# Kernel tuning notes

Measured on AMD Instinct MI355X. Metric: run time of the kernel, lower is better.

The kernel has to match this reference:

```python
import jax, jax.numpy as jnp
import numpy as np

VOXEL_SIZE = 0.05  # init kwarg


def setup_inputs() -> dict:
    key = jax.random.key(0)
    N, B = 4_194_304, 16
    # coords uniform in [0, 5)^3 -> ~100^3 voxel cells per scene at voxel_size=0.05
    coord = jax.random.uniform(key, (N, 3), dtype=jnp.float32) * 5.0
    # cumulative batch offsets (equal-sized scenes), as pointops expects
    offset = (jnp.arange(1, B + 1, dtype=jnp.int32) * (N // B)).astype(jnp.int32)
    return {"coord": coord, "offset": offset}


def _voxel_mean(coord, offset, voxel_size):
    """Faithful jax port of voxelize_helper + segment_csr(mean) + batch2offset.

    Returns:
      n_p    [N,3]  voxel-mean coords, padded with zeros beyond n_voxels
      n_o    [B]    cumulative voxel counts per batch (batch2offset)
      counts [N]    points per voxel (idx_ptr = concat([0], cumsum(counts[valid])))
    """
    N = coord.shape[0]
    B = offset.shape[0]
    # batch id per point from cumulative offsets
    batch = jnp.searchsorted(offset, jnp.arange(N), side='right')  # [N]
    # start = per-batch min coord (start=None path of voxelize_helper)
    start = jax.ops.segment_min(coord, batch, num_segments=B)      # [B,3]
    grid = jnp.floor((coord - start[batch]) / voxel_size).astype(jnp.int32)  # [N,3]
    G = jnp.max(grid) + 1  # grid extent (per-axis upper bound)
    # linearized cluster key: unique per (batch, gx, gy, gz)
    ckey = ((batch * G + grid[:, 0]) * G + grid[:, 1]) * G + grid[:, 2]
    fill = B * G * G * G  # sentinel beyond any real key
    # sorted unique cluster keys == CSR segment order after sorting cluster indices
    uniq, inv = jnp.unique(ckey, return_inverse=True, size=N, fill_value=fill)
    # fused gather + segment-mean (equivalent to coord[sorted_idx] -> segment_csr mean)
    seg_sum = jax.ops.segment_sum(coord, inv, num_segments=N)                 # [N,3]
    counts = jax.ops.segment_sum(jnp.ones((N,), coord.dtype), inv, num_segments=N)
    n_p = seg_sum / jnp.maximum(counts, 1.0)[:, None]
    # batch id per voxel -> batch2offset (cumulative voxel counts)
    valid = uniq < fill
    vbatch = jnp.where(valid, uniq // (G * G * G), B)
    per_batch = jax.ops.segment_sum(valid.astype(jnp.int32), vbatch, num_segments=B + 1)[:B]
    n_o = jnp.cumsum(per_batch)
    return n_p, n_o, counts.astype(jnp.int32)


def reference(coord, offset):
    return _voxel_mean(coord, offset, VOXEL_SIZE)
```

## Files before the change

### kernel.cpp

```cpp
#include <hip/hip_runtime.h>
#include <stdint.h>


typedef unsigned int uint;
typedef unsigned long long u64;

#define VS 0.05f
#define QSCALE (4096.0f / VS)
#define QINV  (VS / 4096.0f)
#define NBUCKET 2048
#define CPB 16384
#define NBLK_P 256
#define DENSE_MAX 8192

__device__ __forceinline__ uint f2m(float f) {
    uint b = __float_as_uint(f);
    return (b & 0x80000000u) ? ~b : (b | 0x80000000u);
}
__device__ __forceinline__ float m2f(uint m) {
    uint b = (m & 0x80000000u) ? (m & 0x7fffffffu) : ~m;
    return __uint_as_float(b);
}

__global__ void k_init(uint* start_m, int B3) {
    int i = blockIdx.x * blockDim.x + threadIdx.x;
    if (i < B3) start_m[i] = 0xFFFFFFFFu;
}

__global__ void __launch_bounds__(256)
k_minmax(const float* __restrict__ coord, const int* __restrict__ offset,
         int N, int B, uint* start_m) {
    __shared__ uint smin[768];
    __shared__ int soff[256];
    int t = threadIdx.x;
    int nb3 = B * 3;
    for (int j = t; j < B; j += 256) soff[j] = offset[j];
    for (int j = t; j < nb3; j += 256) smin[j] = 0xFFFFFFFFu;
    __syncthreads();

    int F = 3 * N;
    int NQ = F >> 2;
    int per = (NQ + gridDim.x - 1) / gridDim.x;
    int qlo = blockIdx.x * per;
    int qhi = min(NQ, qlo + per);
    const float4* __restrict__ c4 = reinterpret_cast<const float4*>(coord);

    bool fast = false;
    int bU = 0;
    if (qlo < qhi) {
        int pF = (4 * qlo) / 3;
        int pL = (4 * qhi - 1) / 3;
        int bF = 0, bL = 0;
        for (int j = 0; j < B; ++j) {
            bF += (pF >= soff[j]) ? 1 : 0;
            bL += (pL >= soff[j]) ? 1 : 0;
        }
        fast = (bF == bL);
        bU = bF;
    }

    if (fast) {
        int q = qlo + t;
        int p0 = q % 3;
        float s0 = INFINITY, s1 = INFINITY, s2 = INFINITY;
        for (;;) {
            if (q >= qhi) break;
            float4 v = c4[q];
            s0 = fminf(s0, fminf(v.x, v.w)); s1 = fminf(s1, v.y); s2 = fminf(s2, v.z);
            q += 256;
            if (q >= qhi) break;
            v = c4[q];
            s1 = fminf(s1, fminf(v.x, v.w)); s2 = fminf(s2, v.y); s0 = fminf(s0, v.z);
            q += 256;
            if (q >= qhi) break;
            v = c4[q];
            s2 = fminf(s2, fminf(v.x, v.w)); s0 = fminf(s0, v.y); s1 = fminf(s1, v.z);
            q += 256;
        }
        float ax, ay, az;
        if (p0 == 0)      { ax = s0; ay = s1; az = s2; }
        else if (p0 == 1) { ax = s2; ay = s0; az = s1; }
        else              { ax = s1; ay = s2; az = s0; }
        for (int d = 32; d; d >>= 1) {
            ax = fminf(ax, __shfl_xor(ax, d));
            ay = fminf(ay, __shfl_xor(ay, d));
            az = fminf(az, __shfl_xor(az, d));
        }
        if ((t & 63) == 0 && ax < INFINITY) {
            atomicMin(&smin[bU * 3 + 0], f2m(ax));
            atomicMin(&smin[bU * 3 + 1], f2m(ay));
            atomicMin(&smin[bU * 3 + 2], f2m(az));
        }
    } else {
        for (int q = qlo + t; q < qhi; q += 256) {
            float4 v = c4[q];
            int e = 4 * q;
            float vals[4] = {v.x, v.y, v.z, v.w};
#pragma unroll
            for (int k = 0; k < 4; ++k) {
                int ee = e + k;
                int pt = ee / 3;
                int axis = ee - 3 * pt;
                int b = 0;
                for (int j = 0; j < B; ++j) b += (pt >= soff[j]) ? 1 : 0;
                atomicMin(&smin[b * 3 + axis], f2m(vals[k]));
            }
        }
    }

    if (blockIdx.x == 0) {
        for (int ee = 4 * NQ + t; ee < F; ee += 256) {
            int pt = ee / 3;
            int axis = ee - 3 * pt;
            int b = 0;
            for (int j = 0; j < B; ++j) b += (pt >= soff[j]) ? 1 : 0;
            atomicMin(&smin[b * 3 + axis], f2m(coord[ee]));
        }
    }
    __syncthreads();
    for (int j = t; j < nb3; j += 256) {
        uint mn = smin[j];
        if (mn != 0xFFFFFFFFu) atomicMin(&start_m[j], mn);
    }
}

__device__ __forceinline__ void point_grid(const float* __restrict__ coord, int i,
                                           const int* soff, const float* sstart, int B,
                                           float& x, float& y, float& z,
                                           int& b, int& gx, int& gy, int& gz) {
    x = coord[3 * i + 0]; y = coord[3 * i + 1]; z = coord[3 * i + 2];
    b = 0;
    for (int j = 0; j < B; ++j) b += (i >= soff[j]) ? 1 : 0;
    gx = min((int)floorf((x - sstart[b * 3 + 0]) / VS), 127);
    gy = min((int)floorf((y - sstart[b * 3 + 1]) / VS), 127);
    gz = min((int)floorf((z - sstart[b * 3 + 2]) / VS), 127);
}

__device__ __forceinline__ u64 frac12(float x, float y, float z,
                                      const float* sstart, int b,
                                      int gx, int gy, int gz) {
    float fx = fmaxf(x - (sstart[b * 3 + 0] + (float)gx * VS), 0.0f);
    float fy = fmaxf(y - (sstart[b * 3 + 1] + (float)gy * VS), 0.0f);
    float fz = fmaxf(z - (sstart[b * 3 + 2] + (float)gz * VS), 0.0f);
    uint ux = min((uint)(fx * QSCALE + 0.5f), 4095u);
    uint uy = min((uint)(fy * QSCALE + 0.5f), 4095u);
    uint uz = min((uint)(fz * QSCALE + 0.5f), 4095u);
    return ((u64)ux << 24) | ((u64)uy << 12) | (u64)uz;
}


__global__ void __launch_bounds__(1024)
k_count(const float* __restrict__ coord, const int* __restrict__ offset,
        int N, int B, const uint* __restrict__ start_m, uint* __restrict__ histm) {
    __shared__ uint hist[NBUCKET];
    __shared__ int soff[16];
    __shared__ float sstart[48];
    int t = threadIdx.x;
    if (t < B) soff[t] = offset[t];
    if (t < B * 3) sstart[t] = m2f(start_m[t]);
    for (int j = t; j < NBUCKET; j += blockDim.x) hist[j] = 0;
    __syncthreads();
    int chunk = (N + gridDim.x - 1) / gridDim.x;
    int lo = blockIdx.x * chunk, hi = min(N, lo + chunk);
    for (int i = lo + t; i < hi; i += blockDim.x) {
        float x, y, z; int b, gx, gy, gz;
        point_grid(coord, i, soff, sstart, B, x, y, z, b, gx, gy, gz);
        atomicAdd(&hist[(b << 7) | gx], 1u);
    }
    __syncthreads();
    for (int j = t; j < NBUCKET; j += blockDim.x)
        histm[(size_t)j * NBLK_P + blockIdx.x] = hist[j];
}

__global__ void k_scanrow(uint* __restrict__ histm, uint* __restrict__ tot) {
    __shared__ uint sc[256];
    uint* row = histm + (size_t)blockIdx.x * NBLK_P;
    int t = threadIdx.x;
    uint v = row[t];
    sc[t] = v;
    __syncthreads();
    for (int d = 1; d < 256; d <<= 1) {
        uint add = (t >= d) ? sc[t - d] : 0;
        __syncthreads();
        sc[t] += add;
        __syncthreads();
    }
    row[t] = sc[t] - v;
    if (t == 255) tot[blockIdx.x] = sc[255];
}

__global__ void k_scan2048(const uint* __restrict__ in, uint* __restrict__ out) {
    __shared__ uint p[1024];
    int t = threadIdx.x;
    uint a = in[2 * t], bb = in[2 * t + 1];
    p[t] = a + bb;
    __syncthreads();
    for (int d = 1; d < 1024; d <<= 1) {
        uint add = (t >= d) ? p[t - d] : 0;
        __syncthreads();
        p[t] += add;
        __syncthreads();
    }
    uint ex = p[t] - (a + bb);
    out[2 * t] = ex;
    out[2 * t + 1] = ex + a;
    if (t == 1023) out[2048] = p[1023];
}

__global__ void __launch_bounds__(1024)
k_partition(const float* __restrict__ coord, const int* __restrict__ offset,
            int N, int B, const uint* __restrict__ start_m,
            const uint* __restrict__ histm, const uint* __restrict__ bucket_base,
            u64* __restrict__ recs) {
    __shared__ uint cursor[NBUCKET];
    __shared__ int soff[16];
    __shared__ float sstart[48];
    int t = threadIdx.x;
    if (t < B) soff[t] = offset[t];
    if (t < B * 3) sstart[t] = m2f(start_m[t]);
    for (int j = t; j < NBUCKET; j += blockDim.x)
        cursor[j] = bucket_base[j] + histm[(size_t)j * NBLK_P + blockIdx.x];
    __syncthreads();
    int chunk = (N + gridDim.x - 1) / gridDim.x;
    int lo = blockIdx.x * chunk, hi = min(N, lo + chunk);
    for (int i = lo + t; i < hi; i += blockDim.x) {
        float x, y, z; int b, gx, gy, gz;
        point_grid(coord, i, soff, sstart, B, x, y, z, b, gx, gy, gz);
        uint cell = ((uint)gy << 7) | (uint)gz;
        u64 rec = ((u64)cell << 36) | frac12(x, y, z, sstart, b, gx, gy, gz);
        uint slot = atomicAdd(&cursor[(b << 7) | gx], 1u);
        recs[slot] = rec;
    }
}

__global__ void k_vox(const u64* __restrict__ recs, const uint* __restrict__ bucket_base,
                      uint* __restrict__ voxcount, uint* __restrict__ gmask) {
    __shared__ uint bits[512];
    __shared__ uint wsum[4];
    int q = blockIdx.x;
    uint lo = bucket_base[q], hi = bucket_base[q + 1];
    for (int j = threadIdx.x; j < 512; j += blockDim.x) bits[j] = 0;
    __syncthreads();
    for (uint i = lo + threadIdx.x; i < hi; i += blockDim.x) {
        uint c = (uint)(recs[i] >> 36);
        atomicOr(&bits[c >> 5], 1u << (c & 31));
    }
    __syncthreads();
    uint s = 0;
    for (int w = threadIdx.x; w < 512; w += blockDim.x) {
        uint m = bits[w];
        gmask[(size_t)q * 512 + w] = m;
        s += __popc(m);
    }
    for (int d = 32; d; d >>= 1) s += __shfl_xor(s, d);
    if ((threadIdx.x & 63) == 0) wsum[threadIdx.x >> 6] = s;
    __syncthreads();
    if (threadIdx.x == 0) voxcount[q] = wsum[0] + wsum[1] + wsum[2] + wsum[3];
}

__global__ void k_no3(const uint* __restrict__ voxscan, int B, float* __restrict__ no_out) {
    int t = threadIdx.x;
    if (t < B) no_out[t] = (float)voxscan[(t + 1) << 7];
}

__global__ void k_tailzero(const uint* __restrict__ voxscan, int N, int B, int out_total,
                           float* __restrict__ np_out, float* __restrict__ cnt_out,
                           float* __restrict__ out) {
    uint total = voxscan[NBUCKET];
    int stride = gridDim.x * blockDim.x;
    int tid = blockIdx.x * blockDim.x + threadIdx.x;
    for (int j = 3 * (int)total + tid; j < 3 * N; j += stride) np_out[j] = 0.0f;
    for (int j = (int)total + tid; j < N; j += stride) cnt_out[j] = 0.0f;
    for (int j = 4 * N + B + tid; j < out_total; j += stride) out[j] = 0.0f;
}

__global__ void __launch_bounds__(1024)
k_emit2(const u64* __restrict__ recs, const uint* __restrict__ bucket_base,
        const uint* __restrict__ voxscan, const uint* __restrict__ gmask,
        const uint* __restrict__ start_m, float* __restrict__ np_out,
        float* __restrict__ cnt_out) {
    __shared__ u64 dense[DENSE_MAX];
    __shared__ uint mask[512], wrank[512];
    __shared__ uint svc;
    __shared__ float sstart[48];
    int q = blockIdx.x;
    uint lo = bucket_base[q], hi = bucket_base[q + 1];
    if (lo == hi) return;
    int t = threadIdx.x;
    if (t < 48) sstart[t] = m2f(start_m[t]);
    if (t < 512) {
        uint m = gmask[(size_t)q * 512 + t];
        mask[t] = m;
        wrank[t] = __popc(m);
    }
    __syncthreads();
    for (int d = 1; d < 512; d <<= 1) {
        uint add = (t < 512 && t >= d) ? wrank[t - d] : 0;
        __syncthreads();
        if (t < 512) wrank[t] += add;
        __syncthreads();
    }
    if (t == 511) svc = wrank[511];
    if (t < 512) wrank[t] -= __popc(mask[t]);
    __syncthreads();
    uint vc = svc;
    uint base_r = voxscan[q];
    int b = q >> 7, gx = q & 127;
    float cx = sstart[b * 3 + 0] + (float)gx * VS;
    float sy = sstart[b * 3 + 1], sz = sstart[b * 3 + 2];
    for (uint segbase = 0; segbase < vc; segbase += DENSE_MAX) {
        uint seglen = min(vc - segbase, (uint)DENSE_MAX);
        for (uint j = t; j < seglen; j += 1024) dense[j] = 0ull;
        __syncthreads();
        for (uint i = lo + t; i < hi; i += 1024) {
            u64 rec = recs[i];
            uint c = (uint)(rec >> 36);
            uint w = c >> 5, bit = c & 31;
            uint r = wrank[w] + __popc(mask[w] & ((1u << bit) - 1u));
            if (r >= segbase && r < segbase + seglen) {
                u64 enc = (((rec >> 24) & 0xFFFull) << 46) | (((rec >> 12) & 0xFFFull) << 28)
                        | ((rec & 0xFFFull) << 10) | 1ull;
                atomicAdd(&dense[r - segbase], enc);
            }
        }
        __syncthreads();
        for (uint rr = segbase + t; rr < segbase + seglen; rr += 1024) {
            uint l2 = 0, h2 = 511;
            while (l2 < h2) {
                uint mid = (l2 + h2 + 1) >> 1;
                if (wrank[mid] <= rr) l2 = mid; else h2 = mid - 1;
            }
            uint w = l2;
            uint idx = rr - wrank[w];
            uint m = mask[w], bit = 0, c;
            c = __popc(m & 0xFFFFu); if (idx >= c) { idx -= c; bit += 16; m >>= 16; }
            c = __popc(m & 0xFFu);   if (idx >= c) { idx -= c; bit += 8;  m >>= 8; }
            c = __popc(m & 0xFu);    if (idx >= c) { idx -= c; bit += 4;  m >>= 4; }
            c = __popc(m & 0x3u);    if (idx >= c) { idx -= c; bit += 2;  m >>= 2; }
            c = __popc(m & 0x1u);    if (idx >= c) { bit += 1; }
            uint cell = (w << 5) + bit;
            uint gy = cell >> 7, gz = cell & 127u;
            u64 p = dense[rr - segbase];
            float cnt = (float)(uint)(p & 1023ull);
            float inv = 1.0f / fmaxf(cnt, 1.0f);
            uint uz = (uint)((p >> 10) & 0x3FFFFull);
            uint uy = (uint)((p >> 28) & 0x3FFFFull);
            uint ux = (uint)(p >> 46);
            uint r_out = base_r + rr;
            np_out[3 * r_out + 0] = cx + ((float)ux * QINV) * inv;
            np_out[3 * r_out + 1] = sy + (float)gy * VS + ((float)uy * QINV) * inv;
            np_out[3 * r_out + 2] = sz + (float)gz * VS + ((float)uz * QINV) * inv;
            cnt_out[r_out] = cnt;
        }
        __syncthreads();
    }
}


__global__ void k_hist(const float* __restrict__ coord, const int* __restrict__ offset,
                       int N, int B, const uint* __restrict__ start_m,
                       uint* __restrict__ mask) {
    __shared__ int soff[256];
    __shared__ float sstart[768];
    for (int j = threadIdx.x; j < B; j += blockDim.x) soff[j] = offset[j];
    for (int j = threadIdx.x; j < B * 3; j += blockDim.x) sstart[j] = m2f(start_m[j]);
    __syncthreads();
    int i = blockIdx.x * blockDim.x + threadIdx.x;
    if (i >= N) return;
    float x, y, z; int b, gx, gy, gz;
    point_grid(coord, i, soff, sstart, B, x, y, z, b, gx, gy, gz);
    uint key = ((uint)b << 21) | ((uint)gx << 14) | ((uint)gy << 7) | (uint)gz;
    atomicOr(&mask[key >> 5], 1u << (key & 31));
}

__global__ void k_scan1(const uint* __restrict__ mask, uint* __restrict__ partial) {
    int base = blockIdx.x * 1024 + threadIdx.x * 4;
    uint4 m = *(const uint4*)(mask + base);
    uint s = __popc(m.x) + __popc(m.y) + __popc(m.z) + __popc(m.w);
    for (int d = 32; d; d >>= 1) s += __shfl_xor(s, d);
    __shared__ uint wsum[4];
    if ((threadIdx.x & 63) == 0) wsum[threadIdx.x >> 6] = s;
    __syncthreads();
    if (threadIdx.x == 0) partial[blockIdx.x] = wsum[0] + wsum[1] + wsum[2] + wsum[3];
}

__global__ void k_scan2(uint* partial, int P, uint* total) {
    __shared__ uint t[256];
    uint carry = 0;
    for (int base = 0; base < P; base += 256) {
        int j = base + threadIdx.x;
        uint v = (j < P) ? partial[j] : 0;
        t[threadIdx.x] = v;
        __syncthreads();
        for (int d = 1; d < 256; d <<= 1) {
            uint add = (threadIdx.x >= d) ? t[threadIdx.x - d] : 0;
            __syncthreads();
            t[threadIdx.x] += add;
            __syncthreads();
        }
        uint inc = t[threadIdx.x];
        uint chunk = t[255];
        if (j < P) partial[j] = carry + inc - v;
        __syncthreads();
        carry += chunk;
    }
    if (threadIdx.x == 0) *total = carry;
}

__global__ void k_scan3(const uint* __restrict__ mask, const uint* __restrict__ partial,
                        uint* __restrict__ wordrank) {
    int base = blockIdx.x * 1024 + threadIdx.x * 4;
    uint4 m = *(const uint4*)(mask + base);
    uint c0 = __popc(m.x), c1 = __popc(m.y), c2 = __popc(m.z), c3 = __popc(m.w);
    uint s = c0 + c1 + c2 + c3;
    __shared__ uint t[256];
    t[threadIdx.x] = s;
    __syncthreads();
    for (int d = 1; d < 256; d <<= 1) {
        uint add = (threadIdx.x >= d) ? t[threadIdx.x - d] : 0;
        __syncthreads();
        t[threadIdx.x] += add;
        __syncthreads();
    }
    uint ex = t[threadIdx.x] - s + partial[blockIdx.x];
    uint4 r;
    r.x = ex; r.y = ex + c0; r.z = ex + c0 + c1; r.w = ex + c0 + c1 + c2;
    *(uint4*)(wordrank + base) = r;
}

__global__ void k_no(const uint* mask, const uint* wordrank, const uint* total,
                     float* no_out, int B, int W) {
    int b = blockIdx.x * blockDim.x + threadIdx.x;
    if (b >= B) return;
    long long idx = (long long)(b + 1) << 21;
    uint w = (uint)(idx >> 5);
    uint v;
    if (w >= (uint)W) v = *total;
    else v = wordrank[w];
    no_out[b] = (float)v;
}

__global__ void k_accum_sparse(const float* __restrict__ coord, const int* __restrict__ offset,
                               int N, int B, const uint* __restrict__ start_m,
                               const uint* __restrict__ mask, const uint* __restrict__ wordrank,
                               u64* __restrict__ packed) {
    __shared__ int soff[256];
    __shared__ float sstart[768];
    for (int j = threadIdx.x; j < B; j += blockDim.x) soff[j] = offset[j];
    for (int j = threadIdx.x; j < B * 3; j += blockDim.x) sstart[j] = m2f(start_m[j]);
    __syncthreads();
    int i = blockIdx.x * blockDim.x + threadIdx.x;
    if (i >= N) return;
    float x, y, z; int b, gx, gy, gz;
    point_grid(coord, i, soff, sstart, B, x, y, z, b, gx, gy, gz);
    uint key = ((uint)b << 21) | ((uint)gx << 14) | ((uint)gy << 7) | (uint)gz;
    uint w = key >> 5, bit = key & 31;
    uint r = wordrank[w] + __popc(mask[w] & ((1u << bit) - 1u));
    u64 f = frac12(x, y, z, sstart, b, gx, gy, gz);
    u64 enc = (((f >> 24) & 0xFFFull) << 46) | (((f >> 12) & 0xFFFull) << 28)
            | ((f & 0xFFFull) << 10) | 1ull;
    atomicAdd(&packed[r], enc);
}

__global__ void k_decode_sparse(const uint* __restrict__ mask, const uint* __restrict__ wordrank,
                                const uint* __restrict__ start_m,
                                const u64* __restrict__ packed, int W,
                                float* __restrict__ np_out, float* __restrict__ cnt_out) {
    __shared__ float sstart[48];
    for (int j = threadIdx.x; j < 48; j += blockDim.x) sstart[j] = m2f(start_m[j]);
    __syncthreads();
    int w = blockIdx.x * blockDim.x + threadIdx.x;
    if (w >= W) return;
    uint m = mask[w];
    if (m == 0) return;
    uint r = wordrank[w];
    uint kbase = (uint)w << 5;
    while (m) {
        uint bit = (uint)__ffs(m) - 1u;
        m &= m - 1u;
        uint key = kbase + bit;
        u64 p = packed[r];
        float cnt = (float)(uint)(p & 1023ull);
        float inv = 1.0f / fmaxf(cnt, 1.0f);
        uint uz = (uint)((p >> 10) & 0x3FFFFull);
        uint uy = (uint)((p >> 28) & 0x3FFFFull);
        uint ux = (uint)(p >> 46);
        uint b = key >> 21;
        uint gx = (key >> 14) & 127u;
        uint gy = (key >> 7) & 127u;
        uint gz = key & 127u;
        np_out[3 * r + 0] = sstart[b * 3 + 0] + (float)gx * VS + ((float)ux * QINV) * inv;
        np_out[3 * r + 1] = sstart[b * 3 + 1] + (float)gy * VS + ((float)uy * QINV) * inv;
        np_out[3 * r + 2] = sstart[b * 3 + 2] + (float)gz * VS + ((float)uz * QINV) * inv;
        cnt_out[r] = cnt;
        ++r;
    }
}

extern "C" void kernel_launch(void* const* d_in, const int* in_sizes, int n_in,
                              void* d_out, int out_size, void* d_ws, size_t ws_size,
                              hipStream_t stream) {
    const float* coord = (const float*)d_in[0];
    const int* offset = (const int*)d_in[1];
    int N = in_sizes[0] / 3;
    int B = in_sizes[1];

    float* out = (float*)d_out;
    float* np_out = out;
    float* no_out = out + (size_t)3 * N;
    float* cnt_out = no_out + B;

    uint8_t* base = (uint8_t*)d_ws;
    uint* start_m = (uint*)base;
    uint* total = start_m + (size_t)B * 3;

    uintptr_t p = (uintptr_t)(total + 1);
    p = (p + 255) & ~(uintptr_t)255;
    uint* histm = (uint*)p;          p += (size_t)NBUCKET * NBLK_P * 4;
    p = (p + 255) & ~(uintptr_t)255;
    uint* tot = (uint*)p;            p += (size_t)NBUCKET * 4;
    p = (p + 255) & ~(uintptr_t)255;
    uint* bucket_base = (uint*)p;    p += (size_t)(NBUCKET + 1) * 4;
    p = (p + 255) & ~(uintptr_t)255;
    uint* voxcount = (uint*)p;       p += (size_t)NBUCKET * 4;
    p = (p + 255) & ~(uintptr_t)255;
    uint* voxscan = (uint*)p;        p += (size_t)(NBUCKET + 1) * 4;
    p = (p + 255) & ~(uintptr_t)255;
    uint* gmask = (uint*)p;          p += (size_t)NBUCKET * 512 * 4;
    p = (p + 255) & ~(uintptr_t)255;
    u64* recs = (u64*)p;             p += (size_t)N * 8;
    size_t need_part = p - (uintptr_t)base;

    k_init<<<(B * 3 + 255) / 256, 256, 0, stream>>>(start_m, B * 3);
    k_minmax<<<2048, 256, 0, stream>>>(coord, offset, N, B, start_m);

    if (B <= 16 && ws_size >= need_part) {
        k_count<<<NBLK_P, 1024, 0, stream>>>(coord, offset, N, B, start_m, histm);
        k_scanrow<<<NBUCKET, 256, 0, stream>>>(histm, tot);
        k_scan2048<<<1, 1024, 0, stream>>>(tot, bucket_base);
        k_partition<<<NBLK_P, 1024, 0, stream>>>(coord, offset, N, B, start_m, histm,
                                                 bucket_base, recs);
        k_vox<<<NBUCKET, 256, 0, stream>>>(recs, bucket_base, voxcount, gmask);
        k_scan2048<<<1, 1024, 0, stream>>>(voxcount, voxscan);
        k_no3<<<1, 64, 0, stream>>>(voxscan, B, no_out);
        k_tailzero<<<1024, 256, 0, stream>>>(voxscan, N, B, out_size,
                                             np_out, cnt_out, out);
        k_emit2<<<NBUCKET, 1024, 0, stream>>>(recs, bucket_base, voxscan, gmask,
                                              start_m, np_out, cnt_out);
    } else {
        hipMemsetAsync(d_out, 0, (size_t)out_size * sizeof(float), stream);
        size_t W = (size_t)B << 16;
        int nblk1 = (int)(W / 1024);
        uintptr_t sp = (uintptr_t)(total + 1);
        sp = (sp + 255) & ~(uintptr_t)255;
        uint* partial = (uint*)sp;   sp += (size_t)nblk1 * 4;
        sp = (sp + 255) & ~(uintptr_t)255;
        uint* mask = (uint*)sp;      sp += W * 4;
        sp = (sp + 255) & ~(uintptr_t)255;
        uint* wordrank = (uint*)sp;  sp += W * 4;
        sp = (sp + 255) & ~(uintptr_t)255;
        u64* packed = (u64*)sp;
        int nb = (N + 255) / 256;
        hipMemsetAsync(mask, 0, W * sizeof(uint), stream);
        hipMemsetAsync(packed, 0, (size_t)N * sizeof(u64), stream);
        k_hist<<<nb, 256, 0, stream>>>(coord, offset, N, B, start_m, mask);
        k_scan1<<<nblk1, 256, 0, stream>>>(mask, partial);
        k_scan2<<<1, 256, 0, stream>>>(partial, nblk1, total);
        k_scan3<<<nblk1, 256, 0, stream>>>(mask, partial, wordrank);
        k_no<<<(B + 63) / 64, 64, 0, stream>>>(mask, wordrank, total, no_out, B, (int)W);
        k_accum_sparse<<<nb, 256, 0, stream>>>(coord, offset, N, B, start_m, mask,
                                               wordrank, packed);
        k_decode_sparse<<<(int)((W + 255) / 256), 256, 0, stream>>>(mask, wordrank, start_m,
                                                                    packed, (int)W,
                                                                    np_out, cnt_out);
    }
}
```

Measured before the change: 206.6 us.

## Fuse voxel occupancy into partition, merge tail-zero into emit, vectorize coord loads

Voxel bitmask construction and per-bucket voxel counting move into the partition kernel, using global atomicOr on gmask plus per-block new-voxel counters. This removes the separate k_vox pass over the records. The gmask and voxcount zeroing is folded into k_scanrow, k_no3 is folded into the second scan, and tail zeroing runs as extra blocks of k_emit2, which cuts the launch count. Count and partition load coordinates as float4 when a block's chunk lies in a single batch, and the in-block rank scan in emit uses wavefront shuffles. The cost is many global atomics on gmask during partition.

After: 338.9 us. 1.64x slower.

```diff
diff --git a/kernel.cpp b/kernel.cpp
--- a/kernel.cpp
+++ b/kernel.cpp
@@ -9,7 +9,6 @@
 #define QSCALE (4096.0f / VS)
 #define QINV  (VS / 4096.0f)
 #define NBUCKET 2048
-#define CPB 16384
 #define NBLK_P 256
 #define DENSE_MAX 8192
 
@@ -124,30 +123,6 @@
     }
 }
 
-__device__ __forceinline__ void point_grid(const float* __restrict__ coord, int i,
-                                           const int* soff, const float* sstart, int B,
-                                           float& x, float& y, float& z,
-                                           int& b, int& gx, int& gy, int& gz) {
-    x = coord[3 * i + 0]; y = coord[3 * i + 1]; z = coord[3 * i + 2];
-    b = 0;
-    for (int j = 0; j < B; ++j) b += (i >= soff[j]) ? 1 : 0;
-    gx = min((int)floorf((x - sstart[b * 3 + 0]) / VS), 127);
-    gy = min((int)floorf((y - sstart[b * 3 + 1]) / VS), 127);
-    gz = min((int)floorf((z - sstart[b * 3 + 2]) / VS), 127);
-}
-
-__device__ __forceinline__ u64 frac12(float x, float y, float z,
-                                      const float* sstart, int b,
-                                      int gx, int gy, int gz) {
-    float fx = fmaxf(x - (sstart[b * 3 + 0] + (float)gx * VS), 0.0f);
-    float fy = fmaxf(y - (sstart[b * 3 + 1] + (float)gy * VS), 0.0f);
-    float fz = fmaxf(z - (sstart[b * 3 + 2] + (float)gz * VS), 0.0f);
-    uint ux = min((uint)(fx * QSCALE + 0.5f), 4095u);
-    uint uy = min((uint)(fy * QSCALE + 0.5f), 4095u);
-    uint uz = min((uint)(fz * QSCALE + 0.5f), 4095u);
-    return ((u64)ux << 24) | ((u64)uy << 12) | (u64)uz;
-}
-
 
 __global__ void __launch_bounds__(1024)
 k_count(const float* __restrict__ coord, const int* __restrict__ offset,
@@ -158,26 +133,63 @@
     int t = threadIdx.x;
     if (t < B) soff[t] = offset[t];
     if (t < B * 3) sstart[t] = m2f(start_m[t]);
-    for (int j = t; j < NBUCKET; j += blockDim.x) hist[j] = 0;
+    for (int j = t; j < NBUCKET; j += 1024) hist[j] = 0;
     __syncthreads();
     int chunk = (N + gridDim.x - 1) / gridDim.x;
     int lo = blockIdx.x * chunk, hi = min(N, lo + chunk);
-    for (int i = lo + t; i < hi; i += blockDim.x) {
-        float x, y, z; int b, gx, gy, gz;
-        point_grid(coord, i, soff, sstart, B, x, y, z, b, gx, gy, gz);
-        atomicAdd(&hist[(b << 7) | gx], 1u);
-    }
-    __syncthreads();
-    for (int j = t; j < NBUCKET; j += blockDim.x)
+    int bLo = 0, bHi = 0;
+    for (int j = 0; j < B; ++j) {
+        bLo += (lo >= soff[j]) ? 1 : 0;
+        bHi += (hi - 1 >= soff[j]) ? 1 : 0;
+    }
+    if (lo < hi && bLo == bHi && (lo & 3) == 0) {
+        int b = bLo;
+        float sx = sstart[b * 3];
+        int base = b << 7;
+        const float4* __restrict__ c4 = reinterpret_cast<const float4*>(coord);
+        int gEnd = hi >> 2;
+        for (int g = (lo >> 2) + t; g < gEnd; g += 1024) {
+            float4 v0 = c4[3 * g], v1 = c4[3 * g + 1], v2 = c4[3 * g + 2];
+            int gx0 = min((int)floorf((v0.x - sx) / VS), 127);
+            int gx1 = min((int)floorf((v0.w - sx) / VS), 127);
+            int gx2 = min((int)floorf((v1.z - sx) / VS), 127);
+            int gx3 = min((int)floorf((v2.y - sx) / VS), 127);
+            atomicAdd(&hist[base | gx0], 1u);
+            atomicAdd(&hist[base | gx1], 1u);
+            atomicAdd(&hist[base | gx2], 1u);
+            atomicAdd(&hist[base | gx3], 1u);
+        }
+        for (int i = (gEnd << 2) + t; i < hi; i += 1024) {
+            float x = coord[3 * i];
+            int gx = min((int)floorf((x - sx) / VS), 127);
+            atomicAdd(&hist[base | gx], 1u);
+        }
+    } else {
+        for (int i = lo + t; i < hi; i += 1024) {
+            float x = coord[3 * i];
+            int b = 0;
+            for (int j = 0; j < B; ++j) b += (i >= soff[j]) ? 1 : 0;
+            int gx = min((int)floorf((x - sstart[b * 3]) / VS), 127);
+            atomicAdd(&hist[(b << 7) | gx], 1u);
+        }
+    }
+    __syncthreads();
+    for (int j = t; j < NBUCKET; j += 1024)
         histm[(size_t)j * NBLK_P + blockIdx.x] = hist[j];
 }
 
-__global__ void k_scanrow(uint* __restrict__ histm, uint* __restrict__ tot) {
+__global__ void k_scanrow(uint* __restrict__ histm, uint* __restrict__ tot,
+                          uint* __restrict__ gmask, uint* __restrict__ voxcount) {
     __shared__ uint sc[256];
-    uint* row = histm + (size_t)blockIdx.x * NBLK_P;
+    int q = blockIdx.x;
+    uint* row = histm + (size_t)q * NBLK_P;
     int t = threadIdx.x;
     uint v = row[t];
     sc[t] = v;
+    uint* gm = gmask + (size_t)q * 512;
+    gm[t] = 0;
+    gm[t + 256] = 0;
+    if (t == 0) voxcount[q] = 0;
     __syncthreads();
     for (int d = 1; d < 256; d <<= 1) {
         uint add = (t >= d) ? sc[t - d] : 0;
@@ -186,7 +198,7 @@
         __syncthreads();
     }
     row[t] = sc[t] - v;
-    if (t == 255) tot[blockIdx.x] = sc[255];
+    if (t == 255) tot[q] = sc[255];
 }
 
 __global__ void k_scan2048(const uint* __restrict__ in, uint* __restrict__ out) {
@@ -207,103 +219,153 @@
     if (t == 1023) out[2048] = p[1023];
 }
 
+__global__ void k_scan2048b(const uint* __restrict__ in, uint* __restrict__ out,
+                            int B, float* __restrict__ no_out) {
+    __shared__ uint p[1024];
+    int t = threadIdx.x;
+    uint a = in[2 * t], bb = in[2 * t + 1];
+    p[t] = a + bb;
+    __syncthreads();
+    for (int d = 1; d < 1024; d <<= 1) {
+        uint add = (t >= d) ? p[t - d] : 0;
+        __syncthreads();
+        p[t] += add;
+        __syncthreads();
+    }
+    uint ex = p[t] - (a + bb);
+    out[2 * t] = ex;
+    out[2 * t + 1] = ex + a;
+    if (t == 1023) out[2048] = p[1023];
+    if (t < B) no_out[t] = (float)p[((t + 1) << 6) - 1];
+}
+
+__device__ __forceinline__ void part_point(float x, float y, float z, int b,
+                                           float sx, float sy, float sz,
+                                           uint* cursor, uint* newv,
+                                           uint* __restrict__ gmask,
+                                           u64* __restrict__ recs) {
+    int gx = min((int)floorf((x - sx) / VS), 127);
+    int gy = min((int)floorf((y - sy) / VS), 127);
+    int gz = min((int)floorf((z - sz) / VS), 127);
+    float fx = fmaxf(x - (sx + (float)gx * VS), 0.0f);
+    float fy = fmaxf(y - (sy + (float)gy * VS), 0.0f);
+    float fz = fmaxf(z - (sz + (float)gz * VS), 0.0f);
+    uint ux = min((uint)(fx * QSCALE + 0.5f), 4095u);
+    uint uy = min((uint)(fy * QSCALE + 0.5f), 4095u);
+    uint uz = min((uint)(fz * QSCALE + 0.5f), 4095u);
+    uint cell = ((uint)gy << 7) | (uint)gz;
+    u64 rec = ((u64)cell << 36) | ((u64)ux << 24) | ((u64)uy << 12) | (u64)uz;
+    uint q = ((uint)b << 7) | (uint)gx;
+    uint slot = atomicAdd(&cursor[q], 1u);
+    recs[slot] = rec;
+    uint bm = 1u << (cell & 31u);
+    uint old = atomicOr(&gmask[(size_t)q * 512u + (cell >> 5)], bm);
+    if (!(old & bm)) atomicAdd(&newv[q], 1u);
+}
+
 __global__ void __launch_bounds__(1024)
 k_partition(const float* __restrict__ coord, const int* __restrict__ offset,
             int N, int B, const uint* __restrict__ start_m,
             const uint* __restrict__ histm, const uint* __restrict__ bucket_base,
-            u64* __restrict__ recs) {
+            u64* __restrict__ recs, uint* __restrict__ gmask,
+            uint* __restrict__ voxcount) {
     __shared__ uint cursor[NBUCKET];
+    __shared__ uint newv[NBUCKET];
     __shared__ int soff[16];
     __shared__ float sstart[48];
     int t = threadIdx.x;
     if (t < B) soff[t] = offset[t];
     if (t < B * 3) sstart[t] = m2f(start_m[t]);
-    for (int j = t; j < NBUCKET; j += blockDim.x)
+    for (int j = t; j < NBUCKET; j += 1024) {
         cursor[j] = bucket_base[j] + histm[(size_t)j * NBLK_P + blockIdx.x];
+        newv[j] = 0;
+    }
     __syncthreads();
     int chunk = (N + gridDim.x - 1) / gridDim.x;
     int lo = blockIdx.x * chunk, hi = min(N, lo + chunk);
-    for (int i = lo + t; i < hi; i += blockDim.x) {
-        float x, y, z; int b, gx, gy, gz;
-        point_grid(coord, i, soff, sstart, B, x, y, z, b, gx, gy, gz);
-        uint cell = ((uint)gy << 7) | (uint)gz;
-        u64 rec = ((u64)cell << 36) | frac12(x, y, z, sstart, b, gx, gy, gz);
-        uint slot = atomicAdd(&cursor[(b << 7) | gx], 1u);
-        recs[slot] = rec;
-    }
-}
-
-__global__ void k_vox(const u64* __restrict__ recs, const uint* __restrict__ bucket_base,
-                      uint* __restrict__ voxcount, uint* __restrict__ gmask) {
-    __shared__ uint bits[512];
-    __shared__ uint wsum[4];
-    int q = blockIdx.x;
-    uint lo = bucket_base[q], hi = bucket_base[q + 1];
-    for (int j = threadIdx.x; j < 512; j += blockDim.x) bits[j] = 0;
-    __syncthreads();
-    for (uint i = lo + threadIdx.x; i < hi; i += blockDim.x) {
-        uint c = (uint)(recs[i] >> 36);
-        atomicOr(&bits[c >> 5], 1u << (c & 31));
-    }
-    __syncthreads();
-    uint s = 0;
-    for (int w = threadIdx.x; w < 512; w += blockDim.x) {
-        uint m = bits[w];
-        gmask[(size_t)q * 512 + w] = m;
-        s += __popc(m);
-    }
-    for (int d = 32; d; d >>= 1) s += __shfl_xor(s, d);
-    if ((threadIdx.x & 63) == 0) wsum[threadIdx.x >> 6] = s;
-    __syncthreads();
-    if (threadIdx.x == 0) voxcount[q] = wsum[0] + wsum[1] + wsum[2] + wsum[3];
-}
-
-__global__ void k_no3(const uint* __restrict__ voxscan, int B, float* __restrict__ no_out) {
-    int t = threadIdx.x;
-    if (t < B) no_out[t] = (float)voxscan[(t + 1) << 7];
-}
-
-__global__ void k_tailzero(const uint* __restrict__ voxscan, int N, int B, int out_total,
-                           float* __restrict__ np_out, float* __restrict__ cnt_out,
-                           float* __restrict__ out) {
-    uint total = voxscan[NBUCKET];
-    int stride = gridDim.x * blockDim.x;
-    int tid = blockIdx.x * blockDim.x + threadIdx.x;
-    for (int j = 3 * (int)total + tid; j < 3 * N; j += stride) np_out[j] = 0.0f;
-    for (int j = (int)total + tid; j < N; j += stride) cnt_out[j] = 0.0f;
-    for (int j = 4 * N + B + tid; j < out_total; j += stride) out[j] = 0.0f;
+    int bLo = 0, bHi = 0;
+    for (int j = 0; j < B; ++j) {
+        bLo += (lo >= soff[j]) ? 1 : 0;
+        bHi += (hi - 1 >= soff[j]) ? 1 : 0;
+    }
+    if (lo < hi && bLo == bHi && (lo & 3) == 0) {
+        int b = bLo;
+        float sx = sstart[b * 3 + 0], sy = sstart[b * 3 + 1], sz = sstart[b * 3 + 2];
+        const float4* __restrict__ c4 = reinterpret_cast<const float4*>(coord);
+        int gEnd = hi >> 2;
+        for (int g = (lo >> 2) + t; g < gEnd; g += 1024) {
+            float4 v0 = c4[3 * g], v1 = c4[3 * g + 1], v2 = c4[3 * g + 2];
+            part_point(v0.x, v0.y, v0.z, b, sx, sy, sz, cursor, newv, gmask, recs);
+            part_point(v0.w, v1.x, v1.y, b, sx, sy, sz, cursor, newv, gmask, recs);
+            part_point(v1.z, v1.w, v2.x, b, sx, sy, sz, cursor, newv, gmask, recs);
+            part_point(v2.y, v2.z, v2.w, b, sx, sy, sz, cursor, newv, gmask, recs);
+        }
+        for (int i = (gEnd << 2) + t; i < hi; i += 1024) {
+            float x = coord[3 * i + 0], y = coord[3 * i + 1], z = coord[3 * i + 2];
+            part_point(x, y, z, b, sx, sy, sz, cursor, newv, gmask, recs);
+        }
+    } else {
+        for (int i = lo + t; i < hi; i += 1024) {
+            float x = coord[3 * i + 0], y = coord[3 * i + 1], z = coord[3 * i + 2];
+            int b = 0;
+            for (int j = 0; j < B; ++j) b += (i >= soff[j]) ? 1 : 0;
+            part_point(x, y, z, b, sstart[b * 3 + 0], sstart[b * 3 + 1],
+                       sstart[b * 3 + 2], cursor, newv, gmask, recs);
+        }
+    }
+    __syncthreads();
+    for (int j = t; j < NBUCKET; j += 1024) {
+        uint v = newv[j];
+        if (v) atomicAdd(&voxcount[j], v);
+    }
 }
 
 __global__ void __launch_bounds__(1024)
 k_emit2(const u64* __restrict__ recs, const uint* __restrict__ bucket_base,
         const uint* __restrict__ voxscan, const uint* __restrict__ gmask,
-        const uint* __restrict__ start_m, float* __restrict__ np_out,
-        float* __restrict__ cnt_out) {
+        const uint* __restrict__ start_m, int N, int B, int out_total,
+        float* __restrict__ np_out, float* __restrict__ cnt_out,
+        float* __restrict__ out) {
+    int t = threadIdx.x;
+    if (blockIdx.x >= NBUCKET) {
+        uint total = voxscan[NBUCKET];
+        int zb = blockIdx.x - NBUCKET;
+        int stride = (gridDim.x - NBUCKET) * 1024;
+        int tid = zb * 1024 + t;
+        for (int j = 3 * (int)total + tid; j < 3 * N; j += stride) np_out[j] = 0.0f;
+        for (int j = (int)total + tid; j < N; j += stride) cnt_out[j] = 0.0f;
+        for (int j = 4 * N + B + tid; j < out_total; j += stride) out[j] = 0.0f;
+        return;
+    }
     __shared__ u64 dense[DENSE_MAX];
     __shared__ uint mask[512], wrank[512];
-    __shared__ uint svc;
+    __shared__ uint wtot[8], woff[9];
     __shared__ float sstart[48];
     int q = blockIdx.x;
     uint lo = bucket_base[q], hi = bucket_base[q + 1];
     if (lo == hi) return;
-    int t = threadIdx.x;
     if (t < 48) sstart[t] = m2f(start_m[t]);
+    uint m = 0, c = 0;
     if (t < 512) {
-        uint m = gmask[(size_t)q * 512 + t];
+        m = gmask[(size_t)q * 512 + t];
         mask[t] = m;
-        wrank[t] = __popc(m);
-    }
-    __syncthreads();
-    for (int d = 1; d < 512; d <<= 1) {
-        uint add = (t < 512 && t >= d) ? wrank[t - d] : 0;
-        __syncthreads();
-        if (t < 512) wrank[t] += add;
-        __syncthreads();
-    }
-    if (t == 511) svc = wrank[511];
-    if (t < 512) wrank[t] -= __popc(mask[t]);
-    __syncthreads();
-    uint vc = svc;
+        c = __popc(m);
+    }
+    uint sc = c;
+    for (int d = 1; d < 64; d <<= 1) {
+        uint nb = __shfl_up(sc, d, 64);
+        if ((t & 63) >= d) sc += nb;
+    }
+    if (t < 512 && (t & 63) == 63) wtot[t >> 6] = sc;
+    __syncthreads();
+    if (t == 0) {
+        uint r = 0;
+        for (int k = 0; k < 8; ++k) { woff[k] = r; r += wtot[k]; }
+        woff[8] = r;
+    }
+    __syncthreads();
+    if (t < 512) wrank[t] = sc - c + woff[t >> 6];
+    uint vc = woff[8];
     uint base_r = voxscan[q];
     int b = q >> 7, gx = q & 127;
     float cx = sstart[b * 3 + 0] + (float)gx * VS;
@@ -314,8 +376,8 @@
         __syncthreads();
         for (uint i = lo + t; i < hi; i += 1024) {
             u64 rec = recs[i];
-            uint c = (uint)(rec >> 36);
-            uint w = c >> 5, bit = c & 31;
+            uint cc = (uint)(rec >> 36);
+            uint w = cc >> 5, bit = cc & 31;
             uint r = wrank[w] + __popc(mask[w] & ((1u << bit) - 1u));
             if (r >= segbase && r < segbase + seglen) {
                 u64 enc = (((rec >> 24) & 0xFFFull) << 46) | (((rec >> 12) & 0xFFFull) << 28)
@@ -332,12 +394,12 @@
             }
             uint w = l2;
             uint idx = rr - wrank[w];
-            uint m = mask[w], bit = 0, c;
-            c = __popc(m & 0xFFFFu); if (idx >= c) { idx -= c; bit += 16; m >>= 16; }
-            c = __popc(m & 0xFFu);   if (idx >= c) { idx -= c; bit += 8;  m >>= 8; }
-            c = __popc(m & 0xFu);    if (idx >= c) { idx -= c; bit += 4;  m >>= 4; }
-            c = __popc(m & 0x3u);    if (idx >= c) { idx -= c; bit += 2;  m >>= 2; }
-            c = __popc(m & 0x1u);    if (idx >= c) { bit += 1; }
+            uint mm = mask[w], bit = 0, cp;
+            cp = __popc(mm & 0xFFFFu); if (idx >= cp) { idx -= cp; bit += 16; mm >>= 16; }
+            cp = __popc(mm & 0xFFu);   if (idx >= cp) { idx -= cp; bit += 8;  mm >>= 8; }
+            cp = __popc(mm & 0xFu);    if (idx >= cp) { idx -= cp; bit += 4;  mm >>= 4; }
+            cp = __popc(mm & 0x3u);    if (idx >= cp) { idx -= cp; bit += 2;  mm >>= 2; }
+            cp = __popc(mm & 0x1u);    if (idx >= cp) { bit += 1; }
             uint cell = (w << 5) + bit;
             uint gy = cell >> 7, gz = cell & 127u;
             u64 p = dense[rr - segbase];
@@ -356,6 +418,30 @@
     }
 }
 
+
+__device__ __forceinline__ void point_grid(const float* __restrict__ coord, int i,
+                                           const int* soff, const float* sstart, int B,
+                                           float& x, float& y, float& z,
+                                           int& b, int& gx, int& gy, int& gz) {
+    x = coord[3 * i + 0]; y = coord[3 * i + 1]; z = coord[3 * i + 2];
+    b = 0;
+    for (int j = 0; j < B; ++j) b += (i >= soff[j]) ? 1 : 0;
+    gx = min((int)floorf((x - sstart[b * 3 + 0]) / VS), 127);
+    gy = min((int)floorf((y - sstart[b * 3 + 1]) / VS), 127);
+    gz = min((int)floorf((z - sstart[b * 3 + 2]) / VS), 127);
+}
+
+__device__ __forceinline__ u64 frac12(float x, float y, float z,
+                                      const float* sstart, int b,
+                                      int gx, int gy, int gz) {
+    float fx = fmaxf(x - (sstart[b * 3 + 0] + (float)gx * VS), 0.0f);
+    float fy = fmaxf(y - (sstart[b * 3 + 1] + (float)gy * VS), 0.0f);
+    float fz = fmaxf(z - (sstart[b * 3 + 2] + (float)gz * VS), 0.0f);
+    uint ux = min((uint)(fx * QSCALE + 0.5f), 4095u);
+    uint uy = min((uint)(fy * QSCALE + 0.5f), 4095u);
+    uint uz = min((uint)(fz * QSCALE + 0.5f), 4095u);
+    return ((u64)ux << 24) | ((u64)uy << 12) | (u64)uz;
+}
 
 __global__ void k_hist(const float* __restrict__ coord, const int* __restrict__ offset,
                        int N, int B, const uint* __restrict__ start_m,
@@ -536,17 +622,14 @@
 
     if (B <= 16 && ws_size >= need_part) {
         k_count<<<NBLK_P, 1024, 0, stream>>>(coord, offset, N, B, start_m, histm);
-        k_scanrow<<<NBUCKET, 256, 0, stream>>>(histm, tot);
+        k_scanrow<<<NBUCKET, 256, 0, stream>>>(histm, tot, gmask, voxcount);
         k_scan2048<<<1, 1024, 0, stream>>>(tot, bucket_base);
         k_partition<<<NBLK_P, 1024, 0, stream>>>(coord, offset, N, B, start_m, histm,
-                                                 bucket_base, recs);
-        k_vox<<<NBUCKET, 256, 0, stream>>>(recs, bucket_base, voxcount, gmask);
-        k_scan2048<<<1, 1024, 0, stream>>>(voxcount, voxscan);
-        k_no3<<<1, 64, 0, stream>>>(voxscan, B, no_out);
-        k_tailzero<<<1024, 256, 0, stream>>>(voxscan, N, B, out_size,
-                                             np_out, cnt_out, out);
-        k_emit2<<<NBUCKET, 1024, 0, stream>>>(recs, bucket_base, voxscan, gmask,
-                                              start_m, np_out, cnt_out);
+                                                 bucket_base, recs, gmask, voxcount);
+        k_scan2048b<<<1, 1024, 0, stream>>>(voxcount, voxscan, B, no_out);
+        k_emit2<<<NBUCKET + 1024, 1024, 0, stream>>>(recs, bucket_base, voxscan, gmask,
+                                                     start_m, N, B, out_size,
+                                                     np_out, cnt_out, out);
     } else {
         hipMemsetAsync(d_out, 0, (size_t)out_size * sizeof(float), stream);
         size_t W = (size_t)B << 16;
```
